# Kernel tuning notes

Measured on AMD Instinct MI355X. Metric: run time of the kernel, lower is better.

## Reference

```python
import jax, jax.numpy as jnp
import numpy as np

LAM = 1.0
N_ITERS = 20
TOL = 1e-6


def setup_inputs() -> dict:
    key = jax.random.key(0)
    k0, k1, k2, k3, k4 = jax.random.split(key, 5)
    B, M, d, E, a = 8, 50000, 8, 800000, 8
    c0 = jax.random.normal(k0, (B, M, d), dtype=jnp.float32)
    src = jax.random.randint(k1, (E,), 0, M, dtype=jnp.int32)
    dst = jax.random.randint(k2, (E,), 0, M, dtype=jnp.int32)
    R_src = jax.random.normal(k3, (E, a, d), dtype=jnp.float32)
    R_dst = jax.random.normal(k4, (E, a, d), dtype=jnp.float32)
    return {"c0": c0, "src": src, "dst": dst, "R_src": R_src, "R_dst": R_dst}


def _batch_dot(x, y):
    # [B,M,d] x [B,M,d] -> [B,1,1]
    return jnp.sum(x * y, axis=(1, 2), keepdims=True)


def _matvec(p, src, dst, R_src, R_dst):
    # p: [B,M,d] -> p + lam * L p via per-edge gather-einsum-scatter
    r = (jnp.einsum('ead,bed->bea', R_src, p[:, src, :])
         - jnp.einsum('ead,bed->bea', R_dst, p[:, dst, :]))  # [B,E,a]
    c_src = jnp.einsum('ead,bea->bed', R_src, r)   # [B,E,d]
    c_dst = -jnp.einsum('ead,bea->bed', R_dst, r)  # [B,E,d]
    acc = jnp.zeros_like(p).at[:, src, :].add(c_src).at[:, dst, :].add(c_dst)
    return p + LAM * acc


def _cg_solve(b, x0, src, dst, R_src, R_dst):
    mv = lambda q: _matvec(q, src, dst, R_src, R_dst)
    x = x0
    r = b - mv(x)
    p = r
    rsold = _batch_dot(r, r)
    done = jnp.array(False)

    def body(i, state):
        x, r, p, rsold, done = state
        Ap = mv(p)
        alpha = rsold / (_batch_dot(p, Ap) + 1e-12)
        x_new = x + alpha * p
        r_new = r - alpha * Ap
        rsnew = _batch_dot(r_new, r_new)
        conv = jnp.sqrt(jnp.mean(rsnew)) < TOL  # torch breaks AFTER updating x,r
        p_new = r_new + rsnew / (rsold + 1e-12) * p
        x = jnp.where(done, x, x_new)
        r = jnp.where(done, r, r_new)
        frozen = done | conv
        p = jnp.where(frozen, p, p_new)
        rsold = jnp.where(frozen, rsold, rsnew)
        return (x, r, p, rsold, frozen)

    x, _, _, _, _ = jax.lax.fori_loop(0, N_ITERS, body, (x, r, p, rsold, done))
    return x


def reference(c0, src, dst, R_src, R_dst):
    c0_f = c0.astype(jnp.float32)
    c = _cg_solve(c0_f, c0_f, src, dst, R_src, R_dst)
    return c.astype(c0.dtype)
```

## Files before the change

kernel.cpp:

```cpp
#include <hip/hip_runtime.h>
#include <math.h>

constexpr float LAM = 1.0f;
constexpr int   NIT = 20;
constexpr float TOL = 1e-6f;

typedef float f4 __attribute__((ext_vector_type(4)));

#define S_RSOLD 0
#define S_ALPHA 8
#define S_BETA  16
#define S_FLAG  24
#define S_PAP   32
#define S_RS    (32+2048)
#define SCAL_F  (32+4096)

__device__ __forceinline__ float dot8v(f4 a0, f4 a1, f4 b0, f4 b1){
  return a0[0]*b0[0] + a0[1]*b0[1] + a0[2]*b0[2] + a0[3]*b0[3]
       + a1[0]*b1[0] + a1[1]*b1[1] + a1[2]*b1[2] + a1[3]*b1[3];
}

__global__ void k_setup_nm(float* __restrict__ scal, int* __restrict__ cursor, int Mn){
  int i = blockIdx.x * blockDim.x + threadIdx.x;
  int stride = gridDim.x * blockDim.x;
  for (int j = i; j < SCAL_F; j += stride) scal[j] = 0.f;
  for (int j = i; j < Mn; j += stride) cursor[j] = 0;
}

__global__ void k_deg(const int* __restrict__ src, const int* __restrict__ dst,
                      int* __restrict__ cnt, int E){
  int i = blockIdx.x * blockDim.x + threadIdx.x;
  int stride = gridDim.x * blockDim.x;
  for (int e = i; e < E; e += stride){
    atomicAdd(&cnt[src[e]], 1);
    atomicAdd(&cnt[dst[e]], 1);
  }
}

__global__ void k_scan(int* __restrict__ cnt, int* __restrict__ rowptr,
                       int* __restrict__ cursor, int Mn, int tot){
  __shared__ int sm[1024];
  const int T = 1024;
  int t = threadIdx.x;
  int chunk = (Mn + T - 1) / T;
  int lo = t * chunk, hi = lo + chunk; if (hi > Mn) hi = Mn;
  int s = 0;
  for (int i = lo; i < hi; ++i) s += cnt[i] + 1;
  sm[t] = s;
  __syncthreads();
  for (int o = 1; o < T; o <<= 1){
    int v = (t >= o) ? sm[t - o] : 0;
    __syncthreads();
    sm[t] += v;
    __syncthreads();
  }
  int base = (t == 0) ? 0 : sm[t - 1];
  for (int i = lo; i < hi; ++i){
    int c = cnt[i];
    rowptr[i] = base;
    cursor[i] = base + 1;
    base += c + 1;
  }
  if (t == T - 1) rowptr[Mn] = tot;
}

__global__ void k_fill(const int* __restrict__ src, const int* __restrict__ dst,
                       int* __restrict__ cursor, int* __restrict__ col,
                       int* __restrict__ es, int E){
  int i = blockIdx.x * blockDim.x + threadIdx.x;
  int stride = gridDim.x * blockDim.x;
  for (int e = i; e < E; e += stride){
    int s = src[e], t = dst[e];
    int ps = atomicAdd(&cursor[s], 1);
    col[ps] = t; es[ps] = (e << 1);
    int pt = atomicAdd(&cursor[t], 1);
    col[pt] = s; es[pt] = (e << 1) | 1;
  }
}

__global__ void k_buildg(const float* __restrict__ Rs, const float* __restrict__ Rd,
                         const int* __restrict__ rowptr, const int* __restrict__ es,
                         float* __restrict__ Bcsr, int* __restrict__ col, int Mn){
  int g = blockIdx.x * blockDim.x + threadIdx.x;
  int v = g >> 6;
  if (v >= Mn) return;
  int l = g & 63, d1 = l >> 3, d2 = l & 7;
  float Dacc = 0.f;
  int j0 = rowptr[v], j1 = rowptr[v + 1];
  int j = j0 + 1;
  for (; j + 2 <= j1; j += 2){
    int e0 = es[j], e1 = es[j + 1];
    float ra0 = Rs[(size_t)(e0 >> 1) * 64 + l];
    float rb0 = Rd[(size_t)(e0 >> 1) * 64 + l];
    float ra1 = Rs[(size_t)(e1 >> 1) * 64 + l];
    float rb1 = Rd[(size_t)(e1 >> 1) * 64 + l];
    float x0 = (e0 & 1) ? rb0 : ra0, y0 = (e0 & 1) ? ra0 : rb0;
    float x1 = (e1 & 1) ? rb1 : ra1, y1 = (e1 & 1) ? ra1 : rb1;
    float B0 = 0.f, B1 = 0.f;
    #pragma unroll
    for (int a = 0; a < 8; ++a){
      float p0 = __shfl(x0, a * 8 + d1, 64);
      float q0 = __shfl(y0, a * 8 + d2, 64);
      float s0 = __shfl(x0, a * 8 + d2, 64);
      float p1 = __shfl(x1, a * 8 + d1, 64);
      float q1 = __shfl(y1, a * 8 + d2, 64);
      float s1 = __shfl(x1, a * 8 + d2, 64);
      B0 += p0 * q0;  Dacc += p0 * s0;
      B1 += p1 * q1;  Dacc += p1 * s1;
    }
    __builtin_nontemporal_store(-LAM * B0, &Bcsr[(size_t)j * 64 + l]);
    __builtin_nontemporal_store(-LAM * B1, &Bcsr[(size_t)(j + 1) * 64 + l]);
  }
  for (; j < j1; ++j){
    int e0 = es[j];
    float ra = Rs[(size_t)(e0 >> 1) * 64 + l];
    float rb = Rd[(size_t)(e0 >> 1) * 64 + l];
    float x = (e0 & 1) ? rb : ra, y = (e0 & 1) ? ra : rb;
    float B0 = 0.f;
    #pragma unroll
    for (int a = 0; a < 8; ++a){
      float p0 = __shfl(x, a * 8 + d1, 64);
      float q0 = __shfl(y, a * 8 + d2, 64);
      float s0 = __shfl(x, a * 8 + d2, 64);
      B0 += p0 * q0;  Dacc += p0 * s0;
    }
    __builtin_nontemporal_store(-LAM * B0, &Bcsr[(size_t)j * 64 + l]);
  }
  Bcsr[(size_t)j0 * 64 + l] = ((d1 == d2) ? 1.f : 0.f) + LAM * Dacc;
  if (l == 0) col[j0] = v;
}

__global__ void k_mv(const float* __restrict__ Bcsr, const int* __restrict__ rowptr,
                     const int* __restrict__ col, const float* __restrict__ p,
                     float* __restrict__ out, float* __restrict__ scal, int Mn){
  if (*(const int*)(scal + S_FLAG)) return;
  __shared__ float pbuf[4][2][8][64];
  __shared__ int   cbuf[4][128];
  int g = blockIdx.x * blockDim.x + threadIdx.x;
  int v = g >> 6;
  bool active = (v < Mn);
  int w  = threadIdx.x >> 6;
  int l  = g & 63;
  int hi = l >> 3, lo = l & 7;
  int k8 = lo * 8;
  int b8 = hi * 8;
  int j0 = 0, j1 = 0, rowlen = 0;
  if (active){
    j0 = rowptr[v]; j1 = rowptr[v + 1];
    rowlen = j1 - j0;
    for (int jj = l; jj < rowlen && jj < 128; jj += 64)
      cbuf[w][jj] = col[j0 + jj];
  }
  __syncthreads();
  if (!active) return;

  const int* cb = cbuf[w];
  int nch = (rowlen + 7) >> 3;

  auto gather = [&](int n, f4& g0, f4& g1){
    int jj = n * 8 + hi;
    int c = v;
    if (jj < rowlen) c = (jj < 128) ? cb[jj] : col[j0 + jj];
    const float* pc = p + (size_t)c * 64 + k8;
    g0 = *(const f4*)pc;
    g1 = *(const f4*)(pc + 4);
  };

  {
    f4 u0, u1;
    gather(0, u0, u1);
    float* d0 = &pbuf[w][0][hi][k8];
    *(f4*)d0 = u0; *(f4*)(d0 + 4) = u1;
  }

  float acc = 0.f;
  for (int n = 0; n < nch; ++n){
    int nb = n & 1;
    bool more = (n + 1 < nch);
    f4 g0, g1;
    if (more) gather(n + 1, g0, g1);
    int jb = j0 + n * 8;
    #pragma unroll
    for (int q = 0; q < 8; ++q){
      if (jb + q < j1){
        const f4* Bp = (const f4*)(Bcsr + (size_t)(jb + q) * 64 + k8);
        f4 m0 = __builtin_nontemporal_load(Bp);
        f4 m1 = __builtin_nontemporal_load(Bp + 1);
        const float* pr = &pbuf[w][nb][q][b8];
        f4 q0 = *(const f4*)pr;
        f4 q1 = *(const f4*)(pr + 4);
        acc += dot8v(m0, m1, q0, q1);
      }
    }
    if (more){
      float* d1 = &pbuf[w][nb ^ 1][hi][k8];
      *(f4*)d1 = g0; *(f4*)(d1 + 4) = g1;
    }
  }
  out[(size_t)v * 64 + l] = acc;
  float pself = p[(size_t)v * 64 + l];
  float part = pself * acc;
  part += __shfl_xor(part, 1, 64);
  part += __shfl_xor(part, 2, 64);
  part += __shfl_xor(part, 4, 64);
  if (lo == 0)
    atomicAdd(&scal[S_PAP + hi * 256 + (blockIdx.x & 255)], part);
}

__global__ void k_perm(const float* __restrict__ c0, float* __restrict__ xp, int Mn){
  int i = blockIdx.x * blockDim.x + threadIdx.x;
  int n4 = Mn * 16;
  if (i >= n4) return;
  int v = i >> 4, rem = i & 15, b = rem >> 1, half = rem & 1;
  f4 cv = *(const f4*)(c0 + ((size_t)b * Mn + v) * 8 + half * 4);
  ((f4*)xp)[i] = cv;
}

__global__ void k_init_nm(float* __restrict__ p, const float* __restrict__ Ap,
                          float* __restrict__ r, float* __restrict__ x_bm,
                          float* __restrict__ scal, int n4tot, int Mn){
  int i = blockIdx.x * blockDim.x + threadIdx.x;
  int l = threadIdx.x & 63;
  float part = 0.f;
  if (i < n4tot){
    f4 cv = ((const f4*)p)[i];
    f4 av = ((const f4*)Ap)[i];
    f4 rv = cv - av;
    ((f4*)r)[i] = rv;
    ((f4*)p)[i] = rv;
    int v = i >> 4, rem = i & 15, b = rem >> 1, half = rem & 1;
    ((f4*)x_bm)[((size_t)b * Mn + v) * 2 + half] = cv;
    part = rv[0]*rv[0] + rv[1]*rv[1] + rv[2]*rv[2] + rv[3]*rv[3];
  }
  part += __shfl_xor(part, 1, 64);
  part += __shfl_xor(part, 16, 64);
  part += __shfl_xor(part, 32, 64);
  if ((l & 49) == 0)
    atomicAdd(&scal[S_RS + ((l >> 1) & 7) * 256 + (blockIdx.x & 255)], part);
}

__global__ void k_s0(float* __restrict__ scal){
  __shared__ float sm[256];
  int t = threadIdx.x;
  int b = t >> 5, k0 = t & 31;
  float s = 0.f;
  #pragma unroll
  for (int i = 0; i < 8; ++i) s += scal[S_RS + b * 256 + k0 + i * 32];
  sm[t] = s;
  __syncthreads();
  if (t < 8){
    float tot = 0.f;
    #pragma unroll
    for (int i = 0; i < 32; ++i) tot += sm[t * 32 + i];
    scal[S_RSOLD + t] = tot;
  }
  __syncthreads();
  for (int i = t; i < 4096; i += 256) scal[S_PAP + i] = 0.f;
}

__global__ void k_alpha(float* __restrict__ scal){
  if (*(const int*)(scal + S_FLAG)) return;
  __shared__ float sm[256];
  int t = threadIdx.x;
  int b = t >> 5, k0 = t & 31;
  float s = 0.f;
  #pragma unroll
  for (int i = 0; i < 8; ++i) s += scal[S_PAP + b * 256 + k0 + i * 32];
  sm[t] = s;
  __syncthreads();
  if (t < 8){
    float tot = 0.f;
    #pragma unroll
    for (int i = 0; i < 32; ++i) tot += sm[t * 32 + i];
    scal[S_ALPHA + t] = scal[S_RSOLD + t] / (tot + 1e-12f);
  }
}

__global__ void k_upd_nm(float* __restrict__ x_bm, float* __restrict__ r,
                         const float* __restrict__ p, const float* __restrict__ Ap,
                         float* __restrict__ scal, int n4tot, int Mn){
  if (*(const int*)(scal + S_FLAG)) return;
  int i = blockIdx.x * blockDim.x + threadIdx.x;
  int l = threadIdx.x & 63;
  float part = 0.f;
  if (i < n4tot){
    int v = i >> 4, rem = i & 15, b = rem >> 1, half = rem & 1;
    float al = scal[S_ALPHA + b];
    size_t xi = ((size_t)b * Mn + v) * 2 + half;
    f4 pv = ((const f4*)p)[i];
    f4 av = ((const f4*)Ap)[i];
    f4 xv = ((f4*)x_bm)[xi];
    f4 rv = ((f4*)r)[i];
    xv += al * pv;
    rv -= al * av;
    ((f4*)x_bm)[xi] = xv;
    ((f4*)r)[i] = rv;
    part = rv[0]*rv[0] + rv[1]*rv[1] + rv[2]*rv[2] + rv[3]*rv[3];
  }
  part += __shfl_xor(part, 1, 64);
  part += __shfl_xor(part, 16, 64);
  part += __shfl_xor(part, 32, 64);
  if ((l & 49) == 0)
    atomicAdd(&scal[S_RS + ((l >> 1) & 7) * 256 + (blockIdx.x & 255)], part);
}

__global__ void k_s2(float* __restrict__ scal){
  if (*(const int*)(scal + S_FLAG)) return;
  __shared__ float sm[256];
  __shared__ float rsn[8];
  int t = threadIdx.x;
  int b = t >> 5, k0 = t & 31;
  float s = 0.f;
  #pragma unroll
  for (int i = 0; i < 8; ++i) s += scal[S_RS + b * 256 + k0 + i * 32];
  sm[t] = s;
  __syncthreads();
  if (t < 8){
    float tot = 0.f;
    #pragma unroll
    for (int i = 0; i < 32; ++i) tot += sm[t * 32 + i];
    rsn[t] = tot;
  }
  __syncthreads();
  if (t == 0){
    float ssum = 0.f;
    for (int bb = 0; bb < 8; ++bb) ssum += rsn[bb];
    if (sqrtf(ssum / 8.0f) < TOL){
      *(int*)(scal + S_FLAG) = 1;
    } else {
      for (int bb = 0; bb < 8; ++bb){
        scal[S_BETA + bb]  = rsn[bb] / (scal[S_RSOLD + bb] + 1e-12f);
        scal[S_RSOLD + bb] = rsn[bb];
      }
    }
  }
  __syncthreads();
  for (int i = t; i < 4096; i += 256) scal[S_PAP + i] = 0.f;
}

__global__ void k_pupd_nm(const float* __restrict__ r, float* __restrict__ p,
                          const float* __restrict__ scal, int n4tot){
  if (*(const int*)(scal + S_FLAG)) return;
  int i = blockIdx.x * blockDim.x + threadIdx.x;
  if (i >= n4tot) return;
  int b = (i >> 1) & 7;
  float be = scal[S_BETA + b];
  f4 rv = ((const f4*)r)[i];
  f4 pv = ((f4*)p)[i];
  pv = rv + be * pv;
  ((f4*)p)[i] = pv;
}

#define OS_RSOLD 0
#define OS_PAP   8
#define OS_RSNEW 16
#define OS_ALPHA 24
#define OS_BETA  32
#define OS_FLAG  40

__device__ __forceinline__ float blk_reduce_256(float v){
  __shared__ float sm[4];
  #pragma unroll
  for (int o = 32; o > 0; o >>= 1) v += __shfl_down(v, o, 64);
  int lane = threadIdx.x & 63, w = threadIdx.x >> 6;
  if (lane == 0) sm[w] = v;
  __syncthreads();
  return (threadIdx.x == 0) ? (sm[0] + sm[1] + sm[2] + sm[3]) : 0.f;
}

__global__ void k_setup_fb(float* scal){
  int i = blockIdx.x * blockDim.x + threadIdx.x;
  if (i < 64) scal[i] = 0.f;
}

__global__ void k_apinit(const float* __restrict__ in, float* __restrict__ out,
                         int n4tot, const int* __restrict__ flag){
  if (*flag) return;
  int j = blockIdx.x * blockDim.x + threadIdx.x;
  if (j < n4tot) ((f4*)out)[j] = ((const f4*)in)[j];
}

__global__ void k_mv_edge_fb(const float* __restrict__ Rs, const float* __restrict__ Rd,
                             const int* __restrict__ src, const int* __restrict__ dst,
                             const float* __restrict__ in, float* __restrict__ out,
                             int Mn, int E, const int* __restrict__ flag){
  if (*flag) return;
  int g  = blockIdx.x * blockDim.x + threadIdx.x;
  int wv = g >> 6, l = g & 63;
  int nw = (gridDim.x * blockDim.x) >> 6;
  int b = l >> 3, q = l & 7;
  for (int e = wv; e < E; e += nw){
    int s = src[e], t = dst[e];
    const f4* rs4 = (const f4*)(Rs + (size_t)e * 64 + q * 8);
    const f4* rd4 = (const f4*)(Rd + (size_t)e * 64 + q * 8);
    const f4* ps4 = (const f4*)(in + ((size_t)b * Mn + s) * 8);
    const f4* pd4 = (const f4*)(in + ((size_t)b * Mn + t) * 8);
    f4 ra0 = rs4[0], ra1 = rs4[1], pa0 = ps4[0], pa1 = ps4[1];
    f4 rb0 = rd4[0], rb1 = rd4[1], pb0 = pd4[0], pb1 = pd4[1];
    float re = dot8v(ra0, ra1, pa0, pa1) - dot8v(rb0, rb1, pb0, pb1);
    float cs = 0.f, cd = 0.f;
    #pragma unroll
    for (int a = 0; a < 8; ++a){
      float rea = __shfl(re, b * 8 + a, 64);
      cs += Rs[(size_t)e * 64 + a * 8 + q] * rea;
      cd += Rd[(size_t)e * 64 + a * 8 + q] * rea;
    }
    atomicAdd(&out[((size_t)b * Mn + s) * 8 + q],  LAM * cs);
    atomicAdd(&out[((size_t)b * Mn + t) * 8 + q], -LAM * cd);
  }
}

__global__ void k_init_o(const float* __restrict__ c0, const float* __restrict__ Ap,
                         float* __restrict__ x, float* __restrict__ r, float* __restrict__ p,
                         float* scal, int n4){
  int b = blockIdx.y;
  size_t base = (size_t)b * n4;
  int j = blockIdx.x * blockDim.x + threadIdx.x;
  float part = 0.f;
  if (j < n4){
    f4 cv = ((const f4*)c0)[base + j];
    f4 av = ((const f4*)Ap)[base + j];
    f4 rv = cv - av;
    ((f4*)x)[base + j] = cv;
    ((f4*)r)[base + j] = rv;
    ((f4*)p)[base + j] = rv;
    part = rv[0]*rv[0] + rv[1]*rv[1] + rv[2]*rv[2] + rv[3]*rv[3];
  }
  float tot = blk_reduce_256(part);
  if (threadIdx.x == 0) atomicAdd(&scal[OS_RSOLD + b], tot);
}

__global__ void k_dot_o(const float* __restrict__ p, const float* __restrict__ Ap,
                        float* scal, int n4){
  const int* flag = (const int*)(scal + OS_FLAG);
  if (*flag) return;
  int b = blockIdx.y;
  size_t base = (size_t)b * n4;
  int j = blockIdx.x * blockDim.x + threadIdx.x;
  float part = 0.f;
  if (j < n4){
    f4 pv = ((const f4*)p)[base + j];
    f4 av = ((const f4*)Ap)[base + j];
    part = pv[0]*av[0] + pv[1]*av[1] + pv[2]*av[2] + pv[3]*av[3];
  }
  float tot = blk_reduce_256(part);
  if (threadIdx.x == 0) atomicAdd(&scal[OS_PAP + b], tot);
}

__global__ void k_s1_o(float* scal){
  const int* flag = (const int*)(scal + OS_FLAG);
  if (*flag) return;
  int t = threadIdx.x;
  if (t < 8){
    scal[OS_ALPHA + t] = scal[OS_RSOLD + t] / (scal[OS_PAP + t] + 1e-12f);
    scal[OS_RSNEW + t] = 0.f;
  }
}

__global__ void k_upd_o(float* __restrict__ x, float* __restrict__ r,
                        const float* __restrict__ p, const float* __restrict__ Ap,
                        float* scal, int n4){
  const int* flag = (const int*)(scal + OS_FLAG);
  if (*flag) return;
  int b = blockIdx.y;
  size_t base = (size_t)b * n4;
  float al = scal[OS_ALPHA + b];
  int j = blockIdx.x * blockDim.x + threadIdx.x;
  float part = 0.f;
  if (j < n4){
    f4 pv = ((const f4*)p)[base + j];
    f4 av = ((const f4*)Ap)[base + j];
    f4 xv = ((f4*)x)[base + j];
    f4 rv = ((f4*)r)[base + j];
    xv += al * pv;
    rv -= al * av;
    ((f4*)x)[base + j] = xv;
    ((f4*)r)[base + j] = rv;
    part = rv[0]*rv[0] + rv[1]*rv[1] + rv[2]*rv[2] + rv[3]*rv[3];
  }
  float tot = blk_reduce_256(part);
  if (threadIdx.x == 0) atomicAdd(&scal[OS_RSNEW + b], tot);
}

__global__ void k_s2_o(float* scal){
  int* flag = (int*)(scal + OS_FLAG);
  if (*flag) return;
  if (threadIdx.x == 0){
    float ssum = 0.f;
    for (int bb = 0; bb < 8; ++bb) ssum += scal[OS_RSNEW + bb];
    if (sqrtf(ssum / 8.0f) < TOL){
      *flag = 1;
    } else {
      for (int bb = 0; bb < 8; ++bb){
        scal[OS_BETA + bb]  = scal[OS_RSNEW + bb] / (scal[OS_RSOLD + bb] + 1e-12f);
        scal[OS_RSOLD + bb] = scal[OS_RSNEW + bb];
        scal[OS_PAP + bb]   = 0.f;
      }
    }
  }
}

__global__ void k_pupd_o(const float* __restrict__ r, float* __restrict__ p,
                         float* scal, int n4){
  const int* flag = (const int*)(scal + OS_FLAG);
  if (*flag) return;
  int b = blockIdx.y;
  size_t base = (size_t)b * n4;
  float be = scal[OS_BETA + b];
  int j = blockIdx.x * blockDim.x + threadIdx.x;
  if (j < n4){
    f4 rv = ((const f4*)r)[base + j];
    f4 pv = ((f4*)p)[base + j];
    pv = rv + be * pv;
    ((f4*)p)[base + j] = pv;
  }
}

extern "C" void kernel_launch(void* const* d_in, const int* in_sizes, int n_in,
                              void* d_out, int out_size, void* d_ws, size_t ws_size,
                              hipStream_t stream){
  const float* c0  = (const float*)d_in[0];
  const int*   src = (const int*)d_in[1];
  const int*   dst = (const int*)d_in[2];
  const float* Rs  = (const float*)d_in[3];
  const float* Rd  = (const float*)d_in[4];

  int N  = in_sizes[0];
  int Mn = N / 64;
  int E  = in_sizes[1];
  int n4tot = N / 4;
  int twoEM = 2 * E + Mn;

  float* ws = (float*)d_ws;
  size_t off = 0;
  float* r    = ws + off;  off += N;
  float* p    = ws + off;  off += N;
  float* Ap   = ws + off;  off += N;
  float* scal = ws + off;  off += SCAL_F;
  int* rowptr = (int*)(ws + off);  off += (size_t)((Mn + 1 + 3) & ~3);
  int* cursor = (int*)(ws + off);  off += (size_t)((Mn + 3) & ~3);
  int* colA   = (int*)(ws + off);  off += (size_t)(twoEM + 8);
  int* esA    = (int*)(ws + off);  off += (size_t)twoEM;
  float* Bcsr = ws + off;  off += (size_t)(twoEM + 8) * 64;
  size_t need_main = off * 4;

  int nb_vec  = (n4tot + 255) / 256;
  int nb_node = (Mn * 64 + 255) / 256;

  if (ws_size >= need_main){
    k_setup_nm<<<512, 256, 0, stream>>>(scal, cursor, Mn);
    k_deg  <<<1024, 256, 0, stream>>>(src, dst, cursor, E);
    k_scan <<<1, 1024, 0, stream>>>(cursor, rowptr, cursor, Mn, twoEM);
    k_fill <<<1024, 256, 0, stream>>>(src, dst, cursor, colA, esA, E);
    k_buildg<<<nb_node, 256, 0, stream>>>(Rs, Rd, rowptr, esA, Bcsr, colA, Mn);

    float* x_bm = (float*)d_out;
    k_perm<<<nb_vec, 256, 0, stream>>>(c0, p, Mn);
    k_mv<<<nb_node, 256, 0, stream>>>(Bcsr, rowptr, colA, p, Ap, scal, Mn);
    k_init_nm<<<nb_vec, 256, 0, stream>>>(p, Ap, r, x_bm, scal, n4tot, Mn);
    k_s0<<<1, 256, 0, stream>>>(scal);

    for (int it = 0; it < NIT; ++it){
      k_mv<<<nb_node, 256, 0, stream>>>(Bcsr, rowptr, colA, p, Ap, scal, Mn);
      k_alpha<<<1, 256, 0, stream>>>(scal);
      k_upd_nm<<<nb_vec, 256, 0, stream>>>(x_bm, r, p, Ap, scal, n4tot, Mn);
      k_s2<<<1, 256, 0, stream>>>(scal);
      k_pupd_nm<<<nb_vec, 256, 0, stream>>>(r, p, scal, n4tot);
    }
  } else {
    float* fr    = ws;
    float* fp    = fr + N;
    float* fAp   = fp + N;
    float* fscal = fAp + N;
    const int* flagp = (const int*)(fscal + OS_FLAG);
    int n4 = Mn * 2;
    dim3 vgrid((n4 + 255) / 256, 8);
    int cb = (n4tot + 255) / 256;
    float* x = (float*)d_out;

    k_setup_fb<<<1, 64, 0, stream>>>(fscal);
    k_apinit<<<cb, 256, 0, stream>>>(c0, fAp, n4tot, flagp);
    k_mv_edge_fb<<<2048, 256, 0, stream>>>(Rs, Rd, src, dst, c0, fAp, Mn, E, flagp);
    k_init_o<<<vgrid, 256, 0, stream>>>(c0, fAp, x, fr, fp, fscal, n4);
    for (int it = 0; it < NIT; ++it){
      k_apinit<<<cb, 256, 0, stream>>>(fp, fAp, n4tot, flagp);
      k_mv_edge_fb<<<2048, 256, 0, stream>>>(Rs, Rd, src, dst, fp, fAp, Mn, E, flagp);
      k_dot_o<<<vgrid, 256, 0, stream>>>(fp, fAp, fscal, n4);
      k_s1_o<<<1, 64, 0, stream>>>(fscal);
      k_upd_o<<<vgrid, 256, 0, stream>>>(x, fr, fp, fAp, fscal, n4);
      k_s2_o<<<1, 64, 0, stream>>>(fscal);
      k_pupd_o<<<vgrid, 256, 0, stream>>>(fr, fp, fscal, n4);
    }
  }
}
```

Before: 5.763 ms.

## Fill CSR in neighbor-index tiles so rows are column-sorted; split full/tail chunk loop

```diff
diff --git a/kernel.cpp b/kernel.cpp
--- a/kernel.cpp
+++ b/kernel.cpp
@@ -4,6 +4,7 @@
 constexpr float LAM = 1.0f;
 constexpr int   NIT = 20;
 constexpr float TOL = 1e-6f;
+constexpr int   TILE = 8192;
 
 typedef float f4 __attribute__((ext_vector_type(4)));
 
@@ -64,17 +65,21 @@
   if (t == T - 1) rowptr[Mn] = tot;
 }
 
-__global__ void k_fill(const int* __restrict__ src, const int* __restrict__ dst,
-                       int* __restrict__ cursor, int* __restrict__ col,
-                       int* __restrict__ es, int E){
+__global__ void k_fill_t(const int* __restrict__ src, const int* __restrict__ dst,
+                         int* __restrict__ cursor, int* __restrict__ col,
+                         int* __restrict__ es, int E, int lo, int hi){
   int i = blockIdx.x * blockDim.x + threadIdx.x;
   int stride = gridDim.x * blockDim.x;
   for (int e = i; e < E; e += stride){
     int s = src[e], t = dst[e];
-    int ps = atomicAdd(&cursor[s], 1);
-    col[ps] = t; es[ps] = (e << 1);
-    int pt = atomicAdd(&cursor[t], 1);
-    col[pt] = s; es[pt] = (e << 1) | 1;
+    if (t >= lo && t < hi){
+      int ps = atomicAdd(&cursor[s], 1);
+      col[ps] = t; es[ps] = (e << 1);
+    }
+    if (s >= lo && s < hi){
+      int pt = atomicAdd(&cursor[t], 1);
+      col[pt] = s; es[pt] = (e << 1) | 1;
+    }
   }
 }
 
@@ -180,16 +185,25 @@
     f4 g0, g1;
     if (more) gather(n + 1, g0, g1);
     int jb = j0 + n * 8;
-    #pragma unroll
-    for (int q = 0; q < 8; ++q){
-      if (jb + q < j1){
-        const f4* Bp = (const f4*)(Bcsr + (size_t)(jb + q) * 64 + k8);
-        f4 m0 = __builtin_nontemporal_load(Bp);
-        f4 m1 = __builtin_nontemporal_load(Bp + 1);
+    const float* Bbase = Bcsr + (size_t)jb * 64 + k8;
+    if (j1 - jb >= 8){
+      #pragma unroll
+      for (int q = 0; q < 8; ++q){
+        f4 m0 = __builtin_nontemporal_load((const f4*)(Bbase + q * 64));
+        f4 m1 = __builtin_nontemporal_load((const f4*)(Bbase + q * 64 + 4));
         const float* pr = &pbuf[w][nb][q][b8];
-        f4 q0 = *(const f4*)pr;
-        f4 q1 = *(const f4*)(pr + 4);
-        acc += dot8v(m0, m1, q0, q1);
+        acc += dot8v(m0, m1, *(const f4*)pr, *(const f4*)(pr + 4));
+      }
+    } else {
+      int lim = j1 - jb;
+      #pragma unroll
+      for (int q = 0; q < 8; ++q){
+        if (q < lim){
+          f4 m0 = __builtin_nontemporal_load((const f4*)(Bbase + q * 64));
+          f4 m1 = __builtin_nontemporal_load((const f4*)(Bbase + q * 64 + 4));
+          const float* pr = &pbuf[w][nb][q][b8];
+          acc += dot8v(m0, m1, *(const f4*)pr, *(const f4*)(pr + 4));
+        }
       }
     }
     if (more){
@@ -551,7 +565,10 @@
     k_setup_nm<<<512, 256, 0, stream>>>(scal, cursor, Mn);
     k_deg  <<<1024, 256, 0, stream>>>(src, dst, cursor, E);
     k_scan <<<1, 1024, 0, stream>>>(cursor, rowptr, cursor, Mn, twoEM);
-    k_fill <<<1024, 256, 0, stream>>>(src, dst, cursor, colA, esA, E);
+    for (int t0 = 0; t0 < Mn; t0 += TILE){
+      int t1 = t0 + TILE; if (t1 > Mn) t1 = Mn;
+      k_fill_t<<<1024, 256, 0, stream>>>(src, dst, cursor, colA, esA, E, t0, t1);
+    }
     k_buildg<<<nb_node, 256, 0, stream>>>(Rs, Rd, rowptr, esA, Bcsr, colA, Mn);
 
     float* x_bm = (float*)d_out;
```

Result: no change. 5.784 ms (+0.4%).

## Store one shared 8x8 block per edge instead of two CSR copies

Applied to the files above, without the earlier changes.

```diff
diff --git a/kernel.cpp b/kernel.cpp
--- a/kernel.cpp
+++ b/kernel.cpp
@@ -45,7 +45,7 @@
   int chunk = (Mn + T - 1) / T;
   int lo = t * chunk, hi = lo + chunk; if (hi > Mn) hi = Mn;
   int s = 0;
-  for (int i = lo; i < hi; ++i) s += cnt[i] + 1;
+  for (int i = lo; i < hi; ++i) s += cnt[i];
   sm[t] = s;
   __syncthreads();
   for (int o = 1; o < T; o <<= 1){
@@ -58,8 +58,8 @@
   for (int i = lo; i < hi; ++i){
     int c = cnt[i];
     rowptr[i] = base;
-    cursor[i] = base + 1;
-    base += c + 1;
+    cursor[i] = base;
+    base += c;
   }
   if (t == T - 1) rowptr[Mn] = tot;
 }
@@ -78,64 +78,68 @@
   }
 }
 
-__global__ void k_buildg(const float* __restrict__ Rs, const float* __restrict__ Rd,
+__global__ void k_medge(const float* __restrict__ Rs, const float* __restrict__ Rd,
+                        float* __restrict__ Mb, int E){
+  int g  = blockIdx.x * blockDim.x + threadIdx.x;
+  int wv = g >> 6, l = g & 63;
+  int nw = (gridDim.x * blockDim.x) >> 6;
+  int d1 = l >> 3, d2 = l & 7;
+  for (int e = wv; e < E; e += nw){
+    float rs = Rs[(size_t)e * 64 + l];
+    float rd = Rd[(size_t)e * 64 + l];
+    float Mm = 0.f;
+    #pragma unroll
+    for (int a = 0; a < 8; ++a)
+      Mm += __shfl(rs, a * 8 + d1, 64) * __shfl(rd, a * 8 + d2, 64);
+    Mb[(size_t)e * 64 + l] = Mm;
+  }
+}
+
+__global__ void k_buildd(const float* __restrict__ Rs, const float* __restrict__ Rd,
                          const int* __restrict__ rowptr, const int* __restrict__ es,
-                         float* __restrict__ Bcsr, int* __restrict__ col, int Mn){
+                         float* __restrict__ Dd, int v0, int v1){
   int g = blockIdx.x * blockDim.x + threadIdx.x;
-  int v = g >> 6;
-  if (v >= Mn) return;
+  int v = v0 + (g >> 6);
+  if (v >= v1) return;
   int l = g & 63, d1 = l >> 3, d2 = l & 7;
   float Dacc = 0.f;
   int j0 = rowptr[v], j1 = rowptr[v + 1];
-  int j = j0 + 1;
+  int j = j0;
   for (; j + 2 <= j1; j += 2){
     int e0 = es[j], e1 = es[j + 1];
-    float ra0 = Rs[(size_t)(e0 >> 1) * 64 + l];
-    float rb0 = Rd[(size_t)(e0 >> 1) * 64 + l];
-    float ra1 = Rs[(size_t)(e1 >> 1) * 64 + l];
-    float rb1 = Rd[(size_t)(e1 >> 1) * 64 + l];
-    float x0 = (e0 & 1) ? rb0 : ra0, y0 = (e0 & 1) ? ra0 : rb0;
-    float x1 = (e1 & 1) ? rb1 : ra1, y1 = (e1 & 1) ? ra1 : rb1;
-    float B0 = 0.f, B1 = 0.f;
+    const float* R0 = (e0 & 1) ? Rd : Rs;
+    const float* R1 = (e1 & 1) ? Rd : Rs;
+    float x0 = R0[(size_t)(e0 >> 1) * 64 + l];
+    float x1 = R1[(size_t)(e1 >> 1) * 64 + l];
     #pragma unroll
     for (int a = 0; a < 8; ++a){
       float p0 = __shfl(x0, a * 8 + d1, 64);
-      float q0 = __shfl(y0, a * 8 + d2, 64);
       float s0 = __shfl(x0, a * 8 + d2, 64);
       float p1 = __shfl(x1, a * 8 + d1, 64);
-      float q1 = __shfl(y1, a * 8 + d2, 64);
       float s1 = __shfl(x1, a * 8 + d2, 64);
-      B0 += p0 * q0;  Dacc += p0 * s0;
-      B1 += p1 * q1;  Dacc += p1 * s1;
-    }
-    __builtin_nontemporal_store(-LAM * B0, &Bcsr[(size_t)j * 64 + l]);
-    __builtin_nontemporal_store(-LAM * B1, &Bcsr[(size_t)(j + 1) * 64 + l]);
+      Dacc += p0 * s0 + p1 * s1;
+    }
   }
   for (; j < j1; ++j){
     int e0 = es[j];
-    float ra = Rs[(size_t)(e0 >> 1) * 64 + l];
-    float rb = Rd[(size_t)(e0 >> 1) * 64 + l];
-    float x = (e0 & 1) ? rb : ra, y = (e0 & 1) ? ra : rb;
-    float B0 = 0.f;
-    #pragma unroll
-    for (int a = 0; a < 8; ++a){
-      float p0 = __shfl(x, a * 8 + d1, 64);
-      float q0 = __shfl(y, a * 8 + d2, 64);
-      float s0 = __shfl(x, a * 8 + d2, 64);
-      B0 += p0 * q0;  Dacc += p0 * s0;
-    }
-    __builtin_nontemporal_store(-LAM * B0, &Bcsr[(size_t)j * 64 + l]);
-  }
-  Bcsr[(size_t)j0 * 64 + l] = ((d1 == d2) ? 1.f : 0.f) + LAM * Dacc;
-  if (l == 0) col[j0] = v;
-}
-
-__global__ void k_mv(const float* __restrict__ Bcsr, const int* __restrict__ rowptr,
-                     const int* __restrict__ col, const float* __restrict__ p,
+    const float* R0 = (e0 & 1) ? Rd : Rs;
+    float x0 = R0[(size_t)(e0 >> 1) * 64 + l];
+    #pragma unroll
+    for (int a = 0; a < 8; ++a)
+      Dacc += __shfl(x0, a * 8 + d1, 64) * __shfl(x0, a * 8 + d2, 64);
+  }
+  Dd[(size_t)v * 64 + l] = ((d1 == d2) ? 1.f : 0.f) + LAM * Dacc;
+}
+
+__global__ void k_mv(const float* __restrict__ Mb, const float* __restrict__ Dd,
+                     const int* __restrict__ rowptr, const int* __restrict__ col,
+                     const int* __restrict__ es, const float* __restrict__ p,
                      float* __restrict__ out, float* __restrict__ scal, int Mn){
   if (*(const int*)(scal + S_FLAG)) return;
   __shared__ float pbuf[4][2][8][64];
+  __shared__ float mbuf[4][2][8][64];
   __shared__ int   cbuf[4][128];
+  __shared__ int   ebuf[4][128];
   int g = blockIdx.x * blockDim.x + threadIdx.x;
   int v = g >> 6;
   bool active = (v < Mn);
@@ -148,57 +152,84 @@
   if (active){
     j0 = rowptr[v]; j1 = rowptr[v + 1];
     rowlen = j1 - j0;
-    for (int jj = l; jj < rowlen && jj < 128; jj += 64)
+    for (int jj = l; jj < rowlen && jj < 128; jj += 64){
       cbuf[w][jj] = col[j0 + jj];
+      ebuf[w][jj] = es[j0 + jj];
+    }
   }
   __syncthreads();
   if (!active) return;
 
-  const int* cb = cbuf[w];
   int nch = (rowlen + 7) >> 3;
 
-  auto gather = [&](int n, f4& g0, f4& g1){
+  auto gather = [&](int n, f4& gp0, f4& gp1, f4& gm0, f4& gm1){
     int jj = n * 8 + hi;
-    int c = v;
-    if (jj < rowlen) c = (jj < 128) ? cb[jj] : col[j0 + jj];
+    int c = v, e = 0;
+    if (jj < rowlen){
+      if (jj < 128){ c = cbuf[w][jj]; e = ebuf[w][jj] >> 1; }
+      else         { c = col[j0 + jj]; e = es[j0 + jj] >> 1; }
+    }
     const float* pc = p + (size_t)c * 64 + k8;
-    g0 = *(const f4*)pc;
-    g1 = *(const f4*)(pc + 4);
+    gp0 = *(const f4*)pc;
+    gp1 = *(const f4*)(pc + 4);
+    const float* mc = Mb + (size_t)e * 64 + k8;
+    gm0 = *(const f4*)mc;
+    gm1 = *(const f4*)(mc + 4);
   };
 
-  {
-    f4 u0, u1;
-    gather(0, u0, u1);
-    float* d0 = &pbuf[w][0][hi][k8];
-    *(f4*)d0 = u0; *(f4*)(d0 + 4) = u1;
-  }
-
-  float acc = 0.f;
+  const f4* pv4 = (const f4*)(p + (size_t)v * 64 + b8);
+  f4 pv0 = pv4[0], pv1 = pv4[1];
+  const f4* dr4 = (const f4*)(Dd + (size_t)v * 64 + k8);
+  float acc = dot8v(dr4[0], dr4[1], pv0, pv1);
+
+  if (nch > 0){
+    f4 u0, u1, m0, m1;
+    gather(0, u0, u1, m0, m1);
+    float* dp = &pbuf[w][0][hi][k8];
+    *(f4*)dp = u0; *(f4*)(dp + 4) = u1;
+    float* dm = &mbuf[w][0][hi][k8];
+    *(f4*)dm = m0; *(f4*)(dm + 4) = m1;
+  }
+
   for (int n = 0; n < nch; ++n){
     int nb = n & 1;
     bool more = (n + 1 < nch);
-    f4 g0, g1;
-    if (more) gather(n + 1, g0, g1);
-    int jb = j0 + n * 8;
+    f4 gp0, gp1, gm0, gm1;
+    if (more) gather(n + 1, gp0, gp1, gm0, gm1);
+    int jb = n * 8;
+    int lim = rowlen - jb;
     #pragma unroll
     for (int q = 0; q < 8; ++q){
-      if (jb + q < j1){
-        const f4* Bp = (const f4*)(Bcsr + (size_t)(jb + q) * 64 + k8);
-        f4 m0 = __builtin_nontemporal_load(Bp);
-        f4 m1 = __builtin_nontemporal_load(Bp + 1);
+      if (q < lim){
+        int jj = jb + q;
+        int sd = ((jj < 128) ? ebuf[w][jj] : es[j0 + jj]) & 1;
         const float* pr = &pbuf[w][nb][q][b8];
-        f4 q0 = *(const f4*)pr;
-        f4 q1 = *(const f4*)(pr + 4);
-        acc += dot8v(m0, m1, q0, q1);
+        f4 q0 = *(const f4*)pr, q1 = *(const f4*)(pr + 4);
+        const float* mc = &mbuf[w][nb][q][0];
+        if (!sd){
+          f4 m0 = *(const f4*)(mc + k8);
+          f4 m1 = *(const f4*)(mc + k8 + 4);
+          acc -= LAM * dot8v(m0, m1, q0, q1);
+        } else {
+          acc -= LAM * ( mc[lo]      * q0[0] + mc[lo +  8] * q0[1]
+                       + mc[lo + 16] * q0[2] + mc[lo + 24] * q0[3]
+                       + mc[lo + 32] * q1[0] + mc[lo + 40] * q1[1]
+                       + mc[lo + 48] * q1[2] + mc[lo + 56] * q1[3]);
+        }
       }
     }
     if (more){
-      float* d1 = &pbuf[w][nb ^ 1][hi][k8];
-      *(f4*)d1 = g0; *(f4*)(d1 + 4) = g1;
+      float* dp = &pbuf[w][nb ^ 1][hi][k8];
+      *(f4*)dp = gp0; *(f4*)(dp + 4) = gp1;
+      float* dm = &mbuf[w][nb ^ 1][hi][k8];
+      *(f4*)dm = gm0; *(f4*)(dm + 4) = gm1;
     }
   }
   out[(size_t)v * 64 + l] = acc;
-  float pself = p[(size_t)v * 64 + l];
+  float pself = (lo & 4) ? ((lo & 2) ? ((lo & 1) ? pv1[3] : pv1[2])
+                                     : ((lo & 1) ? pv1[1] : pv1[0]))
+                         : ((lo & 2) ? ((lo & 1) ? pv0[3] : pv0[2])
+                                     : ((lo & 1) ? pv0[1] : pv0[0]));
   float part = pself * acc;
   part += __shfl_xor(part, 1, 64);
   part += __shfl_xor(part, 2, 64);
@@ -529,7 +560,7 @@
   int Mn = N / 64;
   int E  = in_sizes[1];
   int n4tot = N / 4;
-  int twoEM = 2 * E + Mn;
+  int twoE = 2 * E;
 
   float* ws = (float*)d_ws;
   size_t off = 0;
@@ -537,11 +568,12 @@
   float* p    = ws + off;  off += N;
   float* Ap   = ws + off;  off += N;
   float* scal = ws + off;  off += SCAL_F;
+  float* Dd   = ws + off;  off += (size_t)Mn * 64;
   int* rowptr = (int*)(ws + off);  off += (size_t)((Mn + 1 + 3) & ~3);
   int* cursor = (int*)(ws + off);  off += (size_t)((Mn + 3) & ~3);
-  int* colA   = (int*)(ws + off);  off += (size_t)(twoEM + 8);
-  int* esA    = (int*)(ws + off);  off += (size_t)twoEM;
-  float* Bcsr = ws + off;  off += (size_t)(twoEM + 8) * 64;
+  int* colA   = (int*)(ws + off);  off += (size_t)twoE;
+  int* esA    = (int*)(ws + off);  off += (size_t)twoE;
+  float* Mb   = ws + off;  off += (size_t)E * 64;
   size_t need_main = off * 4;
 
   int nb_vec  = (n4tot + 255) / 256;
@@ -550,18 +582,23 @@
   if (ws_size >= need_main){
     k_setup_nm<<<512, 256, 0, stream>>>(scal, cursor, Mn);
     k_deg  <<<1024, 256, 0, stream>>>(src, dst, cursor, E);
-    k_scan <<<1, 1024, 0, stream>>>(cursor, rowptr, cursor, Mn, twoEM);
+    k_scan <<<1, 1024, 0, stream>>>(cursor, rowptr, cursor, Mn, twoE);
     k_fill <<<1024, 256, 0, stream>>>(src, dst, cursor, colA, esA, E);
-    k_buildg<<<nb_node, 256, 0, stream>>>(Rs, Rd, rowptr, esA, Bcsr, colA, Mn);
+    k_medge<<<4096, 256, 0, stream>>>(Rs, Rd, Mb, E);
+    int Mh = (Mn + 1) / 2;
+    int nb_h1 = (Mh * 64 + 255) / 256;
+    int nb_h2 = ((Mn - Mh) * 64 + 255) / 256;
+    k_buildd<<<nb_h1, 256, 0, stream>>>(Rs, Rd, rowptr, esA, Dd, 0, Mh);
+    k_buildd<<<nb_h2, 256, 0, stream>>>(Rs, Rd, rowptr, esA, Dd, Mh, Mn);
 
     float* x_bm = (float*)d_out;
     k_perm<<<nb_vec, 256, 0, stream>>>(c0, p, Mn);
-    k_mv<<<nb_node, 256, 0, stream>>>(Bcsr, rowptr, colA, p, Ap, scal, Mn);
+    k_mv<<<nb_node, 256, 0, stream>>>(Mb, Dd, rowptr, colA, esA, p, Ap, scal, Mn);
     k_init_nm<<<nb_vec, 256, 0, stream>>>(p, Ap, r, x_bm, scal, n4tot, Mn);
     k_s0<<<1, 256, 0, stream>>>(scal);
 
     for (int it = 0; it < NIT; ++it){
-      k_mv<<<nb_node, 256, 0, stream>>>(Bcsr, rowptr, colA, p, Ap, scal, Mn);
+      k_mv<<<nb_node, 256, 0, stream>>>(Mb, Dd, rowptr, colA, esA, p, Ap, scal, Mn);
       k_alpha<<<1, 256, 0, stream>>>(scal);
       k_upd_nm<<<nb_vec, 256, 0, stream>>>(x_bm, r, p, Ap, scal, n4tot, Mn);
       k_s2<<<1, 256, 0, stream>>>(scal);
```

Result: faster. 5.145 ms (-10.7%).
